# Kernel optimization log

Measured on AMD Instinct MI355X. Metric: run time of the kernel, lower is better.

## Reference

```python
import jax, jax.numpy as jnp
import numpy as np

B, N, D_MODEL, H, D_FF, NB_FEAT = 2, 2048, 512, 8, 2048, 256
DH = D_MODEL // H


def layer_norm(x, g, b, eps=1e-5):
    mu = jnp.mean(x, axis=-1, keepdims=True)
    var = jnp.mean((x - mu) ** 2, axis=-1, keepdims=True)
    return g * (x - mu) / jnp.sqrt(var + eps) + b


def softmax_kernel(data, proj, is_query, eps=1e-4):
    # Performer FAVOR+ positive random features. data: [b,h,n,dh], proj: [m,dh]
    dn = data.shape[-1] ** -0.25
    ratio = proj.shape[0] ** -0.5
    dd = jnp.einsum('bhnd,jd->bhnj', dn * data, proj)
    diag = (jnp.sum(data ** 2, axis=-1, keepdims=True) * 0.5) * (dn ** 2)
    if is_query:
        m = jnp.max(dd, axis=-1, keepdims=True)
    else:
        m = jnp.max(dd)
    return ratio * (jnp.exp(dd - diag - m) + eps)


def setup_inputs() -> dict:
    key = jax.random.key(0)
    ks = jax.random.split(key, 12)
    sd = D_MODEL ** -0.5
    sf = D_FF ** -0.5
    return {
        'x': jax.random.normal(ks[0], (B, N, D_MODEL), jnp.float32),
        'Wq': jax.random.normal(ks[1], (D_MODEL, D_MODEL), jnp.float32) * sd,
        'bq': jnp.zeros((D_MODEL,), jnp.float32),
        'Wk': jax.random.normal(ks[2], (D_MODEL, D_MODEL), jnp.float32) * sd,
        'bk': jnp.zeros((D_MODEL,), jnp.float32),
        'Wv': jax.random.normal(ks[3], (D_MODEL, D_MODEL), jnp.float32) * sd,
        'bv': jnp.zeros((D_MODEL,), jnp.float32),
        'Wo': jax.random.normal(ks[4], (D_MODEL, D_MODEL), jnp.float32) * sd,
        'bo': jnp.zeros((D_MODEL,), jnp.float32),
        'proj': jax.random.normal(ks[5], (NB_FEAT, DH), jnp.float32),
        'W1': jax.random.normal(ks[6], (D_MODEL, D_FF), jnp.float32) * sd,
        'b1': jnp.zeros((D_FF,), jnp.float32),
        'W2': jax.random.normal(ks[7], (D_FF, D_MODEL), jnp.float32) * sf,
        'b2': jnp.zeros((D_MODEL,), jnp.float32),
        'g1': jnp.ones((D_MODEL,), jnp.float32),
        'beta1': jnp.zeros((D_MODEL,), jnp.float32),
        'g2': jnp.ones((D_MODEL,), jnp.float32),
        'beta2': jnp.zeros((D_MODEL,), jnp.float32),
    }


def reference(x, Wq, bq, Wk, bk, Wv, bv, Wo, bo, proj, W1, b1, W2, b2, g1, beta1, g2, beta2):
    b, n, d = x.shape
    heads = lambda W, bias: (x @ W + bias).reshape(b, n, H, DH).transpose(0, 2, 1, 3)  # bhnd
    q = softmax_kernel(heads(Wq, bq), proj, is_query=True)   # [b,h,n,m]
    k = softmax_kernel(heads(Wk, bk), proj, is_query=False)  # [b,h,n,m]
    v = heads(Wv, bv)                                        # [b,h,n,dh]
    # non-causal linear attention
    k_sum = jnp.sum(k, axis=-2)                                   # [b,h,m]
    D_inv = 1.0 / jnp.einsum('bhnf,bhf->bhn', q, k_sum)           # [b,h,n]
    context = jnp.einsum('bhnf,bhne->bhfe', k, v)                 # [b,h,m,dh]
    out = jnp.einsum('bhfe,bhnf,bhn->bhne', context, q, D_inv)    # [b,h,n,dh]
    # output_attentions=True: effective attention matrix (abs, head-mean, detached)
    attn = jnp.einsum('bhnf,bhmf->bhnm', q, k) * D_inv[..., None]
    attn_weight = jax.lax.stop_gradient(jnp.mean(jnp.abs(attn), axis=1))  # [b,n,n]
    out = out.transpose(0, 2, 1, 3).reshape(b, n, d)
    out = out @ Wo + bo
    # NOTE: original module has no residual connections
    h1 = layer_norm(out, g1, beta1)
    ff = jax.nn.relu(h1 @ W1 + b1) @ W2 + b2
    y = layer_norm(ff, g2, beta2)
    return y, attn_weight
```

## Files before the change

kernel.cpp:

```cpp
#include <hip/hip_runtime.h>
#include <math.h>

#define B_SZ   2
#define N_TOK  2048
#define DM     512
#define NH     8
#define DHH    64
#define NF     256
#define DFF    2048
#define HF     2048
#define LDQKV  1536

constexpr float DN_SCALE   = 0.35355339059327373f;
constexpr float DIAG_SCALE = 0.0625f;
constexpr float RATIO      = 0.0625f;
constexpr float FEPS       = 1e-4f;
constexpr float LN_EPS     = 1e-5f;

typedef __attribute__((ext_vector_type(8))) short bf16x8;
typedef __attribute__((ext_vector_type(8))) _Float16 f16x8;
typedef __attribute__((ext_vector_type(4))) float f32x4;

__device__ __forceinline__ short f2b(float f) {
  union { float f; unsigned u; } x; x.f = f;
  unsigned r = (x.u + 0x7fff + ((x.u >> 16) & 1)) >> 16;
  return (short)r;
}
__device__ __forceinline__ float b2f(short s) {
  union { unsigned u; float f; } x; x.u = ((unsigned)(unsigned short)s) << 16;
  return x.f;
}
__device__ __forceinline__ void gload16(const void* g, void* l) {
  __builtin_amdgcn_global_load_lds((const __attribute__((address_space(1))) void*)g,
                                   (__attribute__((address_space(3))) void*)l, 16, 0, 0);
}
__device__ __forceinline__ int swz64(int row, int kbyte) {
  return (row * 128 + kbyte) ^ ((row & 7) << 4);
}
__device__ __forceinline__ float reduce_bmax512(const float* __restrict__ bmax,
                                                float* __restrict__ red) {
  int t = threadIdx.x;
  float m = fmaxf(bmax[t], bmax[t + 256]);
  #pragma unroll
  for (int o = 1; o < 64; o <<= 1) m = fmaxf(m, __shfl_xor(m, o, 64));
  if ((t & 63) == 0) red[t >> 6] = m;
  __syncthreads();
  float r = fmaxf(fmaxf(red[0], red[1]), fmaxf(red[2], red[3]));
  __syncthreads();
  return r;
}

constexpr size_t OFF_CTXP  = 0;
constexpr size_t OFF_QB    = 4194304;
constexpr size_t OFF_OUT2  = 0;
constexpr size_t OFF_FF2   = 0;
constexpr size_t OFF_QFB   = 8388608;
constexpr size_t OFF_KB    = 12582912;
constexpr size_t OFF_QKV   = 16777216;
constexpr size_t OFF_FF1B  = 16777216;
constexpr size_t OFF_AOB   = 20971520;
constexpr size_t OFF_H1B   = 22020096;
constexpr size_t OFF_WOT   = 23068672;
constexpr size_t OFF_W1T   = 23199744;
constexpr size_t OFF_W2T   = 23724032;
constexpr size_t OFF_KSUM  = 24248320;
constexpr size_t OFF_DINV  = 24252416;
constexpr size_t OFF_CTXT  = 24285184;
constexpr size_t OFF_BMAX  = 24416256;
constexpr size_t OFF_ROWC  = 24416832;
constexpr size_t OFF_PART  = 24420928;
constexpr size_t OFF_VSUMP = 24552000;


template<bool RELU, bool OUT_BF16, bool BIAS>
__device__ __forceinline__ void gemm128_tile(short* As, short* Bs, int bx, int by,
                                             const short* __restrict__ A,
                                             const short* __restrict__ Bt,
                                             const float* __restrict__ bias,
                                             void* __restrict__ Cout, int K, int ldC) {
  int tid = threadIdx.x, lane = tid & 63, wave = tid >> 6;
  int wm = wave >> 1, wn = wave & 1;
  int bm = by * 128, bn = bx * 128;
  int srow = tid >> 3, scol = (tid & 7) * 8;
  f32x4 acc[4][4] = {};
  for (int k0 = 0; k0 < K; k0 += 64) {
    #pragma unroll
    for (int c = 0; c < 4; ++c) {
      int r = c * 32 + srow;
      gload16(A + (size_t)(bm + r) * K + k0 + scol, As + c * 2048 + wave * 512);
      gload16(Bt + (size_t)(bn + r) * K + k0 + scol, Bs + c * 2048 + wave * 512);
    }
    __syncthreads();
    #pragma unroll
    for (int kk = 0; kk < 2; ++kk) {
      bf16x8 af[4], bf[4];
      int kq = kk * 32 + (lane >> 4) * 8;
      #pragma unroll
      for (int i = 0; i < 4; ++i)
        af[i] = *(const bf16x8*)&As[(wm * 64 + i * 16 + (lane & 15)) * 64 + kq];
      #pragma unroll
      for (int j = 0; j < 4; ++j)
        bf[j] = *(const bf16x8*)&Bs[(wn * 64 + j * 16 + (lane & 15)) * 64 + kq];
      #pragma unroll
      for (int i = 0; i < 4; ++i)
        #pragma unroll
        for (int j = 0; j < 4; ++j)
          acc[i][j] = __builtin_amdgcn_mfma_f32_16x16x32_bf16(af[i], bf[j], acc[i][j], 0, 0, 0);
    }
    __syncthreads();
  }
  int row0 = bm + wm * 64, col0 = bn + wn * 64;
  #pragma unroll
  for (int i = 0; i < 4; ++i) {
    #pragma unroll
    for (int j = 0; j < 4; ++j) {
      int col = col0 + j * 16 + (lane & 15);
      float bv = BIAS ? bias[col] : 0.f;
      #pragma unroll
      for (int r = 0; r < 4; ++r) {
        int row = row0 + i * 16 + (lane >> 4) * 4 + r;
        float v = acc[i][j][r] + bv;
        if (RELU) v = fmaxf(v, 0.f);
        size_t off = (size_t)row * ldC + col;
        if (OUT_BF16) ((short*)Cout)[off] = f2b(v);
        else          ((float*)Cout)[off] = v;
      }
    }
  }
}

__device__ __forceinline__ void attnw_tile(short* As, short* Bs, int flat, int z,
                                           const short* __restrict__ qb,
                                           const short* __restrict__ kb,
                                           const float* __restrict__ rowc,
                                           float* __restrict__ attnw) {
  int tid = threadIdx.x, lane = tid & 63, wave = tid >> 6;
  int srow = tid >> 3, scol = (tid & 7) * 8;
  int tile = flat >> 4, wi = flat & 15;
  int by = (tile >> 2) * 4 + (wi >> 2);
  int bx = (tile & 3) * 4 + (wi & 3);
  int bm = by * 128, bn = bx * 128;
  const short* Ab = qb + (size_t)z * N_TOK * HF;
  const short* Bb = kb + (size_t)z * N_TOK * HF;
  const float* rc = rowc + (size_t)z * N_TOK;
  float* out = attnw + (size_t)z * N_TOK * N_TOK;
  int wm = wave >> 1, wn = wave & 1;

  f32x4 acc[4][4] = {};
  for (int k0 = 0; k0 < HF; k0 += 64) {
    #pragma unroll
    for (int c = 0; c < 4; ++c) {
      int r = c * 32 + srow;
      gload16(Ab + (size_t)(bm + r) * HF + k0 + scol, As + c * 2048 + wave * 512);
      gload16(Bb + (size_t)(bn + r) * HF + k0 + scol, Bs + c * 2048 + wave * 512);
    }
    __syncthreads();
    #pragma unroll
    for (int kk = 0; kk < 2; ++kk) {
      bf16x8 af[4], bf[4];
      int kq = kk * 32 + (lane >> 4) * 8;
      #pragma unroll
      for (int i = 0; i < 4; ++i)
        af[i] = *(const bf16x8*)&As[(wm * 64 + i * 16 + (lane & 15)) * 64 + kq];
      #pragma unroll
      for (int j = 0; j < 4; ++j)
        bf[j] = *(const bf16x8*)&Bs[(wn * 64 + j * 16 + (lane & 15)) * 64 + kq];
      #pragma unroll
      for (int i = 0; i < 4; ++i)
        #pragma unroll
        for (int j = 0; j < 4; ++j)
          acc[i][j] = __builtin_amdgcn_mfma_f32_16x16x32_bf16(af[i], bf[j], acc[i][j], 0, 0, 0);
    }
    __syncthreads();
  }
  int row0 = bm + wm * 64, col0 = bn + wn * 64;
  #pragma unroll
  for (int i = 0; i < 4; ++i) {
    #pragma unroll
    for (int j = 0; j < 4; ++j) {
      int col = col0 + j * 16 + (lane & 15);
      #pragma unroll
      for (int r = 0; r < 4; ++r) {
        int row = row0 + i * 16 + (lane >> 4) * 4 + r;
        out[(size_t)row * N_TOK + col] = acc[i][j][r] + rc[row];
      }
    }
  }
}

template<bool RELU, bool OUT_BF16>
__device__ __forceinline__ void bn64_tile(short* As, short* Bs, int bn, int bm,
                                          const short* __restrict__ A,
                                          const short* __restrict__ Bt,
                                          const float* __restrict__ bias,
                                          void* __restrict__ Cout, int N, int K) {
  int tid = threadIdx.x, lane = tid & 63, wave = tid >> 6;
  int srow = tid >> 3, scol = (tid & 7) * 8;
  f32x4 acc[2][4] = {};
  for (int k0 = 0; k0 < K; k0 += 64) {
    #pragma unroll
    for (int c = 0; c < 4; ++c)
      gload16(A + (size_t)(bm + c * 32 + srow) * K + k0 + scol, As + c * 2048 + wave * 512);
    #pragma unroll
    for (int c = 0; c < 2; ++c)
      gload16(Bt + (size_t)(bn + c * 32 + srow) * K + k0 + scol, Bs + c * 2048 + wave * 512);
    __syncthreads();
    #pragma unroll
    for (int kk = 0; kk < 2; ++kk) {
      bf16x8 af[2], bf[4];
      int kq = kk * 32 + (lane >> 4) * 8;
      #pragma unroll
      for (int i = 0; i < 2; ++i)
        af[i] = *(const bf16x8*)&As[(wave * 32 + i * 16 + (lane & 15)) * 64 + kq];
      #pragma unroll
      for (int j = 0; j < 4; ++j)
        bf[j] = *(const bf16x8*)&Bs[(j * 16 + (lane & 15)) * 64 + kq];
      #pragma unroll
      for (int i = 0; i < 2; ++i)
        #pragma unroll
        for (int j = 0; j < 4; ++j)
          acc[i][j] = __builtin_amdgcn_mfma_f32_16x16x32_bf16(af[i], bf[j], acc[i][j], 0, 0, 0);
    }
    __syncthreads();
  }
  #pragma unroll
  for (int i = 0; i < 2; ++i) {
    #pragma unroll
    for (int j = 0; j < 4; ++j) {
      int col = bn + j * 16 + (lane & 15);
      float bv = bias[col];
      #pragma unroll
      for (int r = 0; r < 4; ++r) {
        int row = bm + wave * 32 + i * 16 + (lane >> 4) * 4 + r;
        float v = acc[i][j][r] + bv;
        if (RELU) v = fmaxf(v, 0.f);
        if (OUT_BF16) ((short*)Cout)[(size_t)row * N + col] = f2b(v);
        else          ((float*)Cout)[(size_t)row * N + col] = v;
      }
    }
  }
}

__device__ __forceinline__ void pv_tile(short* As, short* Bs, int pid,
                                        const short* __restrict__ qfb,
                                        const short* __restrict__ ctxT,
                                        const float* __restrict__ Dinv,
                                        short* __restrict__ aob) {
  int tid = threadIdx.x, lane = tid & 63, wave = tid >> 6;
  int srow = tid >> 3, scol = (tid & 7) * 8;
  int bx = pid & 15, bh = pid >> 4;
  int b = bh >> 3, h = bh & 7;
  int n0 = bx * 128;

  f32x4 acc[2][4] = {};
  for (int k0 = 0; k0 < NF; k0 += 64) {
    #pragma unroll
    for (int c = 0; c < 4; ++c) {
      int r = c * 32 + srow;
      gload16(qfb + (size_t)(b * N_TOK + n0 + r) * HF + h * NF + k0 + scol,
              As + c * 2048 + wave * 512);
    }
    #pragma unroll
    for (int c = 0; c < 2; ++c) {
      int r = c * 32 + srow;
      gload16(ctxT + (size_t)bh * 16384 + (size_t)r * 256 + k0 + scol,
              Bs + c * 2048 + wave * 512);
    }
    __syncthreads();
    #pragma unroll
    for (int kk = 0; kk < 2; ++kk) {
      bf16x8 af[2], bf[4];
      int kq = kk * 32 + (lane >> 4) * 8;
      #pragma unroll
      for (int i = 0; i < 2; ++i)
        af[i] = *(const bf16x8*)&As[(wave * 32 + i * 16 + (lane & 15)) * 64 + kq];
      #pragma unroll
      for (int j = 0; j < 4; ++j)
        bf[j] = *(const bf16x8*)&Bs[(j * 16 + (lane & 15)) * 64 + kq];
      #pragma unroll
      for (int i = 0; i < 2; ++i)
        #pragma unroll
        for (int j = 0; j < 4; ++j)
          acc[i][j] = __builtin_amdgcn_mfma_f32_16x16x32_bf16(af[i], bf[j], acc[i][j], 0, 0, 0);
    }
    __syncthreads();
  }
  #pragma unroll
  for (int i = 0; i < 2; ++i) {
    #pragma unroll
    for (int j = 0; j < 4; ++j) {
      int e = j * 16 + (lane & 15);
      #pragma unroll
      for (int r = 0; r < 4; ++r) {
        int n = n0 + wave * 32 + i * 16 + (lane >> 4) * 4 + r;
        float dv = Dinv[bh * N_TOK + n];
        aob[(size_t)(b * N_TOK + n) * DM + h * DHH + e] = f2b(acc[i][j][r] * dv);
      }
    }
  }
}


__global__ __launch_bounds__(256)
void gemm_mfma_qkv(const short* __restrict__ A, const short* __restrict__ Bt,
                   float* __restrict__ Cout) {
  __shared__ short As[128 * 64];
  __shared__ short Bs[128 * 64];
  gemm128_tile<false, false, false>(As, Bs, blockIdx.x, blockIdx.y, A, Bt, nullptr,
                                    Cout, DM, LDQKV);
}

__global__ __launch_bounds__(256)
void pv_kernel(const short* __restrict__ qfb, const short* __restrict__ ctxT,
               const float* __restrict__ Dinv, short* __restrict__ aob) {
  __shared__ short As[128 * 64];
  __shared__ short Bs[64 * 64];
  pv_tile(As, Bs, blockIdx.x, qfb, ctxT, Dinv, aob);
}

__global__ __launch_bounds__(256)
void gemm_bn64_wo(const short* __restrict__ A, const short* __restrict__ Bt,
                  const float* __restrict__ bias, float* __restrict__ Cout) {
  __shared__ short As[128 * 64];
  __shared__ short Bs[64 * 64];
  bn64_tile<false, false>(As, Bs, blockIdx.x * 64, blockIdx.y * 128, A, Bt, bias, Cout, DM, DM);
}

__global__ __launch_bounds__(256)
void fatB1_kernel(const short* __restrict__ qb, const short* __restrict__ kb,
                  const float* __restrict__ rowc, float* __restrict__ attnw,
                  const short* __restrict__ h1b, const short* __restrict__ W1t,
                  const float* __restrict__ b1, short* __restrict__ ff1b) {
  __shared__ short As[128 * 64];
  __shared__ short Bs[128 * 64];
  int bid = blockIdx.x;
  if (bid < 256) {
    attnw_tile(As, Bs, bid, 0, qb, kb, rowc, attnw);
  } else {
    int flat = bid - 256;
    gemm128_tile<true, true, true>(As, Bs, flat & 15, flat >> 4, h1b, W1t, b1, ff1b,
                                   DM, DFF);
  }
}

__global__ __launch_bounds__(256)
void fatB2_kernel(const short* __restrict__ qb, const short* __restrict__ kb,
                  const float* __restrict__ rowc, float* __restrict__ attnw,
                  const short* __restrict__ ff1b, const short* __restrict__ W2t,
                  const float* __restrict__ b2, float* __restrict__ ff2) {
  __shared__ short As[128 * 64];
  __shared__ short Bs[128 * 64];
  int bid = blockIdx.x;
  if (bid < 256) {
    attnw_tile(As, Bs, bid, 1, qb, kb, rowc, attnw);
  } else {
    int pid = bid - 256;
    bn64_tile<false, false>(As, Bs, (pid & 7) * 64, (pid >> 3) * 128,
                            ff1b, W2t, b2, ff2, DM, DFF);
  }
}

__global__ void prep_kernel(const float* __restrict__ x, short* __restrict__ xb,
                            const float* Wq, const float* Wk, const float* Wv, const float* Wo,
                            short* Wqt, short* Wkt, short* Wvt, short* Wot,
                            const float* W1, short* W1t, const float* W2, short* W2t) {
  __shared__ float t[64][65];
  int id = blockIdx.x, tid = threadIdx.x;
  if (id >= 768) {
    size_t base = ((size_t)(id - 768) * 256 + tid) * 8;
    #pragma unroll
    for (int u = 0; u < 8; ++u) xb[base + u] = f2b(x[base + u]);
    return;
  }
  const float* W; short* Wt; int K, N, bx, by;
  if (id < 256) {
    int z = id >> 6, sub = id & 63;
    W  = (z == 0) ? Wq : (z == 1) ? Wk : (z == 2) ? Wv : Wo;
    Wt = (z == 0) ? Wqt : (z == 1) ? Wkt : (z == 2) ? Wvt : Wot;
    K = 512; N = 512; bx = sub & 7; by = sub >> 3;
  } else if (id < 512) {
    int sub = id - 256;
    W = W1; Wt = W1t; K = 512; N = 2048; bx = sub & 31; by = sub >> 5;
  } else {
    int sub = id - 512;
    W = W2; Wt = W2t; K = 2048; N = 512; bx = sub & 7; by = sub >> 3;
  }
  int k0 = by * 64, n0 = bx * 64;
  int lx = tid & 63, ly = tid >> 6;
  for (int r = ly; r < 64; r += 4)
    t[r][lx] = W[(size_t)(k0 + r) * N + n0 + lx];
  __syncthreads();
  for (int r = ly; r < 64; r += 4)
    Wt[(size_t)(n0 + r) * K + k0 + lx] = f2b(t[lx][r]);
}

__global__ __launch_bounds__(256)
void feat_mfma_kernel(const float* __restrict__ qkv, const float* __restrict__ bq,
                      const float* __restrict__ bk, const float* __restrict__ proj,
                      short* __restrict__ qfb, short* __restrict__ kbo,
                      float* __restrict__ part, float* __restrict__ bmax) {
  __shared__ short qh[64 * 64], ql[64 * 64];
  __shared__ short ph[128 * 64], pl[128 * 64];
  __shared__ float dpart[64][4];
  __shared__ float diag[64];
  __shared__ float wred[4];
  __shared__ float colp[4][256];
  int t = threadIdx.x;
  bool isq = (blockIdx.z == 0);
  int coff = isq ? 0 : 512;
  const float* bias = isq ? bq : bk;
  short* qout = isq ? qfb : kbo;
  int bh = blockIdx.y, b = bh >> 3, h = bh & 7;
  int n0 = blockIdx.x * 64;
  int lane = t & 63, w = t >> 6, l15 = lane & 15, lq = lane >> 4;

  {
    int r = t >> 2, cg = (t & 3) * 16;
    const float* src = qkv + (size_t)(b * N_TOK + n0 + r) * LDQKV + coff + h * 64 + cg;
    const float* bs = bias + h * 64 + cg;
    float ss = 0.f;
    #pragma unroll
    for (int c2 = 0; c2 < 2; ++c2) {
      f16x8 H, L;
      #pragma unroll
      for (int u = 0; u < 8; ++u) {
        float xv = src[c2 * 8 + u] + bs[c2 * 8 + u];
        ss += xv * xv;
        _Float16 hi = (_Float16)xv;
        H[u] = hi;
        L[u] = (_Float16)(xv - (float)hi);
      }
      int off = swz64(r, cg * 2 + c2 * 16);
      *(f16x8*)((char*)qh + off) = H;
      *(f16x8*)((char*)ql + off) = L;
    }
    dpart[r][t & 3] = ss;
  }
  __syncthreads();
  if (t < 64)
    diag[t] = (dpart[t][0] + dpart[t][1] + dpart[t][2] + dpart[t][3]) * DIAG_SCALE;

  f16x8 ah[2], al[2];
  #pragma unroll
  for (int kk = 0; kk < 2; ++kk) {
    int off = swz64(w * 16 + l15, kk * 64 + lq * 16);
    ah[kk] = *(f16x8*)((char*)qh + off);
    al[kk] = *(f16x8*)((char*)ql + off);
  }

  f32x4 acc[16] = {};
  #pragma unroll
  for (int half = 0; half < 2; ++half) {
    __syncthreads();
    {
      int r = t & 127, cg = (t >> 7) * 32;
      const float* src = proj + (size_t)(half * 128 + r) * DHH + cg;
      #pragma unroll
      for (int c2 = 0; c2 < 4; ++c2) {
        f16x8 H, L;
        #pragma unroll
        for (int u = 0; u < 8; ++u) {
          float xv = src[c2 * 8 + u];
          _Float16 hi = (_Float16)xv;
          H[u] = hi;
          L[u] = (_Float16)(xv - (float)hi);
        }
        int off = swz64(r, cg * 2 + c2 * 16);
        *(f16x8*)((char*)ph + off) = H;
        *(f16x8*)((char*)pl + off) = L;
      }
    }
    __syncthreads();
    #pragma unroll
    for (int jl = 0; jl < 8; ++jl) {
      int row = jl * 16 + l15;
      #pragma unroll
      for (int kk = 0; kk < 2; ++kk) {
        int off = swz64(row, kk * 64 + lq * 16);
        f16x8 bh8 = *(f16x8*)((char*)ph + off);
        f16x8 bl8 = *(f16x8*)((char*)pl + off);
        acc[half * 8 + jl] = __builtin_amdgcn_mfma_f32_16x16x32_f16(ah[kk], bh8, acc[half * 8 + jl], 0, 0, 0);
        acc[half * 8 + jl] = __builtin_amdgcn_mfma_f32_16x16x32_f16(al[kk], bh8, acc[half * 8 + jl], 0, 0, 0);
        acc[half * 8 + jl] = __builtin_amdgcn_mfma_f32_16x16x32_f16(ah[kk], bl8, acc[half * 8 + jl], 0, 0, 0);
      }
    }
  }

  if (isq) {
    #pragma unroll
    for (int r = 0; r < 4; ++r) {
      float mx = -3.4e38f;
      #pragma unroll
      for (int j = 0; j < 16; ++j) mx = fmaxf(mx, acc[j][r]);
      #pragma unroll
      for (int o = 1; o < 16; o <<= 1) mx = fmaxf(mx, __shfl_xor(mx, o, 64));
      int lrow = w * 16 + lq * 4 + r;
      float dg = diag[lrow];
      float ddm = mx * DN_SCALE;
      size_t base = (size_t)(b * N_TOK + n0 + lrow) * HF + h * NF + l15;
      #pragma unroll
      for (int j = 0; j < 16; ++j) {
        float v = RATIO * (expf(acc[j][r] * DN_SCALE - dg - ddm) + FEPS);
        qout[base + j * 16] = f2b(v);
      }
    }
  } else {
    float mxall = -3.4e38f;
    float cs[16];
    #pragma unroll
    for (int j = 0; j < 16; ++j) cs[j] = 0.f;
    #pragma unroll
    for (int r = 0; r < 4; ++r) {
      int lrow = w * 16 + lq * 4 + r;
      float dg = diag[lrow];
      size_t base = (size_t)(b * N_TOK + n0 + lrow) * HF + h * NF + l15;
      #pragma unroll
      for (int j = 0; j < 16; ++j) {
        float a = acc[j][r];
        mxall = fmaxf(mxall, a);
        float e = expf(a * DN_SCALE - dg);
        cs[j] += e;
        qout[base + j * 16] = f2b(e);
      }
    }
    #pragma unroll
    for (int j = 0; j < 16; ++j) {
      cs[j] += __shfl_xor(cs[j], 16, 64);
      cs[j] += __shfl_xor(cs[j], 32, 64);
    }
    if (lq == 0) {
      #pragma unroll
      for (int j = 0; j < 16; ++j) colp[w][j * 16 + l15] = cs[j];
    }
    #pragma unroll
    for (int o = 1; o < 64; o <<= 1) mxall = fmaxf(mxall, __shfl_xor(mxall, o, 64));
    if (lane == 0) wred[w] = mxall;
    __syncthreads();
    part[(size_t)(bh * 32 + blockIdx.x) * 256 + t] =
        colp[0][t] + colp[1][t] + colp[2][t] + colp[3][t];
    if (t == 0)
      bmax[bh * 32 + blockIdx.x] =
          fmaxf(fmaxf(wred[0], wred[1]), fmaxf(wred[2], wred[3])) * DN_SCALE;
  }
}

__global__ __launch_bounds__(256)
void ctx_part_kernel(const short* __restrict__ kb, const float* __restrict__ qkv,
                     const float* __restrict__ bv, float* __restrict__ ctxp,
                     float* __restrict__ vsump) {
  int bh = blockIdx.y, b = bh >> 3, h = bh & 7;
  int ns = blockIdx.z * 128;
  int tid = threadIdx.x;
  if (blockIdx.x == 4) {
    __shared__ float vred[4][64];
    int e = tid & 63, q = tid >> 6;
    float s = 0.f;
    for (int nn = q * 32; nn < q * 32 + 32; ++nn)
      s += qkv[(size_t)(b * N_TOK + ns + nn) * LDQKV + 1024 + h * DHH + e];
    vred[q][e] = s;
    __syncthreads();
    if (tid < 64)
      vsump[((size_t)blockIdx.z * 16 + bh) * 64 + tid] =
          vred[0][tid] + vred[1][tid] + vred[2][tid] + vred[3][tid] + 128.f * bv[h * DHH + tid];
    return;
  }
  int f0 = blockIdx.x * 64;
  __shared__ float kf[32][68];
  __shared__ float vs[32][68];
  int tf = (tid >> 4) * 4, te = (tid & 15) * 4;
  float acc[4][4] = {};
  for (int n0 = ns; n0 < ns + 128; n0 += 32) {
    #pragma unroll
    for (int i = 0; i < 8; i++) {
      int idx = tid + i * 256;
      int nn = idx >> 6, f = idx & 63;
      kf[nn][f] = b2f(kb[(size_t)(b * N_TOK + n0 + nn) * HF + h * NF + f0 + f]);
    }
    #pragma unroll
    for (int i = 0; i < 8; i++) {
      int idx = tid + i * 256;
      int nn = idx >> 6, e = idx & 63;
      vs[nn][e] = qkv[(size_t)(b * N_TOK + n0 + nn) * LDQKV + 1024 + h * DHH + e] + bv[h * DHH + e];
    }
    __syncthreads();
    #pragma unroll
    for (int nn = 0; nn < 32; nn++) {
      float a[4], bb[4];
      #pragma unroll
      for (int i = 0; i < 4; i++) a[i] = kf[nn][tf + i];
      #pragma unroll
      for (int j = 0; j < 4; j++) bb[j] = vs[nn][te + j];
      #pragma unroll
      for (int i = 0; i < 4; i++)
        #pragma unroll
        for (int j = 0; j < 4; j++) acc[i][j] += a[i] * bb[j];
    }
    __syncthreads();
  }
  #pragma unroll
  for (int i = 0; i < 4; i++)
    #pragma unroll
    for (int j = 0; j < 4; j++)
      ctxp[(size_t)blockIdx.z * 262144 + (size_t)bh * 16384 +
           (size_t)(f0 + tf + i) * 64 + te + j] = acc[i][j];
}

__global__ __launch_bounds__(256)
void smallfat_kernel(const float* __restrict__ part, const float* __restrict__ bmax,
                     float* __restrict__ ksum, const float* __restrict__ ctxp,
                     const float* __restrict__ vsump, short* __restrict__ ctxT) {
  __shared__ float T[64][65];
  __shared__ float red[4];
  int t = threadIdx.x;
  float m = reduce_bmax512(bmax, red);
  float s = expf(-m);
  if (blockIdx.x < 16) {
    int bh = blockIdx.x;
    float sum = 0.f;
    #pragma unroll 8
    for (int c = 0; c < 32; ++c) sum += part[(size_t)(bh * 32 + c) * 256 + t];
    ksum[bh * 256 + t] = RATIO * (s * sum + (float)N_TOK * FEPS);
  } else {
    int id = blockIdx.x - 16;
    int ftile = id & 3, bh = id >> 2;
    int e = t & 63, q = t >> 6;
    float vsum_e = 0.f;
    #pragma unroll
    for (int c = 0; c < 16; ++c) vsum_e += vsump[((size_t)c * 16 + bh) * 64 + e];
    #pragma unroll
    for (int i = 0; i < 16; ++i) {
      int fl = i * 4 + q;
      size_t idx = (size_t)bh * 16384 + (size_t)(ftile * 64 + fl) * 64 + e;
      float sum = 0.f;
      #pragma unroll
      for (int c = 0; c < 16; ++c) sum += ctxp[(size_t)c * 262144 + idx];
      T[fl][e] = RATIO * (s * sum + FEPS * vsum_e);
    }
    __syncthreads();
    #pragma unroll
    for (int i = 0; i < 16; ++i) {
      int er = i * 4 + q;
      ctxT[(size_t)bh * 16384 + (size_t)er * 256 + ftile * 64 + e] = f2b(T[e][er]);
    }
  }
}

__global__ __launch_bounds__(256)
void dinvqs_kernel(const short* __restrict__ qfb, const float* __restrict__ ksum,
                   const float* __restrict__ bmax, float* __restrict__ Dinv,
                   float* __restrict__ rowc, short* __restrict__ qb) {
  __shared__ float red[4];
  __shared__ float wsum[4];
  int R = blockIdx.x;
  int b = R >> 11, n = R & 2047;
  int t = threadIdx.x;
  float m = reduce_bmax512(bmax, red);
  float sc = RATIO * expf(-m);
  bf16x8 qv = *(const bf16x8*)(qfb + (size_t)R * HF + t * 8);
  const float* ks = ksum + b * 2048 + t * 8;
  float p = 0.f;
  #pragma unroll
  for (int u = 0; u < 8; ++u) p += b2f(qv[u]) * ks[u];
  #pragma unroll
  for (int o = 1; o < 32; o <<= 1) p += __shfl_xor(p, o, 64);
  float d = 1.0f / p;
  if ((t & 31) == 0) Dinv[(b * NH + (t >> 5)) * N_TOK + n] = d;
  float dv = d * 0.125f;
  float qs = 0.f;
  bf16x8 o8;
  #pragma unroll
  for (int u = 0; u < 8; ++u) {
    float qb_f = b2f(qv[u]) * dv;
    qs += qb_f;
    o8[u] = f2b(qb_f * sc);
  }
  *(bf16x8*)(qb + (size_t)R * HF + t * 8) = o8;
  #pragma unroll
  for (int o = 1; o < 64; o <<= 1) qs += __shfl_xor(qs, o, 64);
  if ((t & 63) == 0) wsum[t >> 6] = qs;
  __syncthreads();
  if (t == 0) rowc[R] = RATIO * FEPS * (wsum[0] + wsum[1] + wsum[2] + wsum[3]);
}

template<bool OUT_BF16>
__global__ void ln_kernel(const float* __restrict__ x, const float* __restrict__ g,
                          const float* __restrict__ beta, void* __restrict__ y) {
  int row = blockIdx.x, t = threadIdx.x;
  __shared__ float red[4];
  __shared__ float bcast[2];
  const float* xr = x + (size_t)row * DM;
  float v0 = xr[t], v1 = xr[t + 256];
  float s = v0 + v1;
  #pragma unroll
  for (int o = 32; o > 0; o >>= 1) s += __shfl_xor(s, o, 64);
  if ((t & 63) == 0) red[t >> 6] = s;
  __syncthreads();
  if (t == 0) bcast[0] = (red[0] + red[1] + red[2] + red[3]) * (1.0f / 512.0f);
  __syncthreads();
  float mean = bcast[0];
  float d0 = v0 - mean, d1 = v1 - mean;
  float s2 = d0 * d0 + d1 * d1;
  #pragma unroll
  for (int o = 32; o > 0; o >>= 1) s2 += __shfl_xor(s2, o, 64);
  if ((t & 63) == 0) red[t >> 6] = s2;
  __syncthreads();
  if (t == 0) bcast[1] = (red[0] + red[1] + red[2] + red[3]) * (1.0f / 512.0f);
  __syncthreads();
  float inv = rsqrtf(bcast[1] + LN_EPS);
  float o0 = g[t] * d0 * inv + beta[t];
  float o1 = g[t + 256] * d1 * inv + beta[t + 256];
  if (OUT_BF16) {
    ((short*)y)[(size_t)row * DM + t] = f2b(o0);
    ((short*)y)[(size_t)row * DM + t + 256] = f2b(o1);
  } else {
    ((float*)y)[(size_t)row * DM + t] = o0;
    ((float*)y)[(size_t)row * DM + t + 256] = o1;
  }
}

extern "C" void kernel_launch(void* const* d_in, const int* in_sizes, int n_in,
                              void* d_out, int out_size, void* d_ws, size_t ws_size,
                              hipStream_t stream) {
  const float* x     = (const float*)d_in[0];
  const float* Wq    = (const float*)d_in[1];
  const float* bq    = (const float*)d_in[2];
  const float* Wk    = (const float*)d_in[3];
  const float* bk    = (const float*)d_in[4];
  const float* Wv    = (const float*)d_in[5];
  const float* bv    = (const float*)d_in[6];
  const float* Wo    = (const float*)d_in[7];
  const float* bo    = (const float*)d_in[8];
  const float* proj  = (const float*)d_in[9];
  const float* W1    = (const float*)d_in[10];
  const float* b1    = (const float*)d_in[11];
  const float* W2    = (const float*)d_in[12];
  const float* b2    = (const float*)d_in[13];
  const float* g1    = (const float*)d_in[14];
  const float* beta1 = (const float*)d_in[15];
  const float* g2    = (const float*)d_in[16];
  const float* beta2 = (const float*)d_in[17];

  float* ws = (float*)d_ws;
  float* y_out = (float*)d_out;
  float* attnw = y_out + (size_t)B_SZ * N_TOK * DM;

  float* ctxp  = ws + OFF_CTXP;
  short* qb    = (short*)(ws + OFF_QB);
  float* out2  = ws + OFF_OUT2;
  float* ff2   = ws + OFF_FF2;
  short* ff1b  = (short*)(ws + OFF_FF1B);
  short* qfb   = (short*)(ws + OFF_QFB);
  short* xb    = (short*)(ws + OFF_QFB);
  short* kb    = (short*)(ws + OFF_KB);
  short* Wqkvt = (short*)(ws + OFF_KB);
  float* QKVlin = ws + OFF_QKV;
  short* aob   = (short*)(ws + OFF_AOB);
  short* h1b   = (short*)(ws + OFF_H1B);
  short* Wot   = (short*)(ws + OFF_WOT);
  short* W1t   = (short*)(ws + OFF_W1T);
  short* W2t   = (short*)(ws + OFF_W2T);
  float* ksum  = ws + OFF_KSUM;
  float* Dinv  = ws + OFF_DINV;
  short* ctxT  = (short*)(ws + OFF_CTXT);
  float* bmax  = ws + OFF_BMAX;
  float* rowc  = ws + OFF_ROWC;
  float* part  = ws + OFF_PART;
  float* vsump = ws + OFF_VSUMP;

  dim3 blk(256);
  int MT = B_SZ * N_TOK;

  prep_kernel<<<1792, blk, 0, stream>>>(x, xb, Wq, Wk, Wv, Wo,
                                        Wqkvt, Wqkvt + 262144, Wqkvt + 524288, Wot,
                                        W1, W1t, W2, W2t);

  gemm_mfma_qkv<<<dim3(LDQKV / 128, MT / 128), blk, 0, stream>>>(xb, Wqkvt, QKVlin);

  feat_mfma_kernel<<<dim3(N_TOK / 64, B_SZ * NH, 2), blk, 0, stream>>>(
      QKVlin, bq, bk, proj, qfb, kb, part, bmax);

  ctx_part_kernel<<<dim3(5, B_SZ * NH, 16), blk, 0, stream>>>(kb, QKVlin, bv, ctxp, vsump);

  smallfat_kernel<<<80, blk, 0, stream>>>(part, bmax, ksum, ctxp, vsump, ctxT);

  dinvqs_kernel<<<MT, blk, 0, stream>>>(qfb, ksum, bmax, Dinv, rowc, qb);

  pv_kernel<<<dim3(N_TOK / 128 * B_SZ * NH), blk, 0, stream>>>(qfb, ctxT, Dinv, aob);

  gemm_bn64_wo<<<dim3(DM / 64, MT / 128), blk, 0, stream>>>(aob, Wot, bo, out2);

  ln_kernel<true><<<MT, blk, 0, stream>>>(out2, g1, beta1, h1b);

  fatB1_kernel<<<768, blk, 0, stream>>>(qb, kb, rowc, attnw, h1b, W1t, b1, ff1b);

  fatB2_kernel<<<512, blk, 0, stream>>>(qb, kb, rowc, attnw, ff1b, W2t, b2, ff2);

  ln_kernel<false><<<MT, blk, 0, stream>>>(ff2, g2, beta2, y_out);
}
```

Before: 217.3 us.

## Double-buffer attention-weight GEMM and merge both batches into one fused launch

Both batches' attention-weight tiles now run in a single fused launch alongside the W1 GEMM. The separate W2 GEMM runs afterwards as its own bn64 kernel. The attention tile loop is double-buffered in LDS, with explicit vmcnt waits and raw barriers so the next K-slice loads while the current one computes. The context-partial kernel's staging loads are vectorized to 8-wide reads with the V bias hoisted. The intent is to hide global-load latency and rebalance the fused launches. In exchange, LDS use per block doubles, which may reduce occupancy.

New measurement: 224.0 us. 3.1% more time.

```diff
diff --git a/kernel.cpp b/kernel.cpp
--- a/kernel.cpp
+++ b/kernel.cpp
@@ -129,65 +129,6 @@
   }
 }
 
-__device__ __forceinline__ void attnw_tile(short* As, short* Bs, int flat, int z,
-                                           const short* __restrict__ qb,
-                                           const short* __restrict__ kb,
-                                           const float* __restrict__ rowc,
-                                           float* __restrict__ attnw) {
-  int tid = threadIdx.x, lane = tid & 63, wave = tid >> 6;
-  int srow = tid >> 3, scol = (tid & 7) * 8;
-  int tile = flat >> 4, wi = flat & 15;
-  int by = (tile >> 2) * 4 + (wi >> 2);
-  int bx = (tile & 3) * 4 + (wi & 3);
-  int bm = by * 128, bn = bx * 128;
-  const short* Ab = qb + (size_t)z * N_TOK * HF;
-  const short* Bb = kb + (size_t)z * N_TOK * HF;
-  const float* rc = rowc + (size_t)z * N_TOK;
-  float* out = attnw + (size_t)z * N_TOK * N_TOK;
-  int wm = wave >> 1, wn = wave & 1;
-
-  f32x4 acc[4][4] = {};
-  for (int k0 = 0; k0 < HF; k0 += 64) {
-    #pragma unroll
-    for (int c = 0; c < 4; ++c) {
-      int r = c * 32 + srow;
-      gload16(Ab + (size_t)(bm + r) * HF + k0 + scol, As + c * 2048 + wave * 512);
-      gload16(Bb + (size_t)(bn + r) * HF + k0 + scol, Bs + c * 2048 + wave * 512);
-    }
-    __syncthreads();
-    #pragma unroll
-    for (int kk = 0; kk < 2; ++kk) {
-      bf16x8 af[4], bf[4];
-      int kq = kk * 32 + (lane >> 4) * 8;
-      #pragma unroll
-      for (int i = 0; i < 4; ++i)
-        af[i] = *(const bf16x8*)&As[(wm * 64 + i * 16 + (lane & 15)) * 64 + kq];
-      #pragma unroll
-      for (int j = 0; j < 4; ++j)
-        bf[j] = *(const bf16x8*)&Bs[(wn * 64 + j * 16 + (lane & 15)) * 64 + kq];
-      #pragma unroll
-      for (int i = 0; i < 4; ++i)
-        #pragma unroll
-        for (int j = 0; j < 4; ++j)
-          acc[i][j] = __builtin_amdgcn_mfma_f32_16x16x32_bf16(af[i], bf[j], acc[i][j], 0, 0, 0);
-    }
-    __syncthreads();
-  }
-  int row0 = bm + wm * 64, col0 = bn + wn * 64;
-  #pragma unroll
-  for (int i = 0; i < 4; ++i) {
-    #pragma unroll
-    for (int j = 0; j < 4; ++j) {
-      int col = col0 + j * 16 + (lane & 15);
-      #pragma unroll
-      for (int r = 0; r < 4; ++r) {
-        int row = row0 + i * 16 + (lane >> 4) * 4 + r;
-        out[(size_t)row * N_TOK + col] = acc[i][j][r] + rc[row];
-      }
-    }
-  }
-}
-
 template<bool RELU, bool OUT_BF16>
 __device__ __forceinline__ void bn64_tile(short* As, short* Bs, int bn, int bm,
                                           const short* __restrict__ A,
@@ -326,37 +267,102 @@
   bn64_tile<false, false>(As, Bs, blockIdx.x * 64, blockIdx.y * 128, A, Bt, bias, Cout, DM, DM);
 }
 
+template<bool RELU, bool OUT_BF16>
 __global__ __launch_bounds__(256)
-void fatB1_kernel(const short* __restrict__ qb, const short* __restrict__ kb,
+void gemm_bn64(const short* __restrict__ A, const short* __restrict__ Bt,
+               const float* __restrict__ bias, void* __restrict__ Cout,
+               int M, int N, int K) {
+  __shared__ short As[128 * 64];
+  __shared__ short Bs[64 * 64];
+  bn64_tile<RELU, OUT_BF16>(As, Bs, blockIdx.x * 64, blockIdx.y * 128, A, Bt, bias, Cout, N, K);
+}
+
+__global__ __launch_bounds__(256)
+void fatC1_kernel(const short* __restrict__ qb, const short* __restrict__ kb,
                   const float* __restrict__ rowc, float* __restrict__ attnw,
                   const short* __restrict__ h1b, const short* __restrict__ W1t,
                   const float* __restrict__ b1, short* __restrict__ ff1b) {
-  __shared__ short As[128 * 64];
-  __shared__ short Bs[128 * 64];
+  __shared__ short As[2][128 * 64];
+  __shared__ short Bs[2][128 * 64];
   int bid = blockIdx.x;
-  if (bid < 256) {
-    attnw_tile(As, Bs, bid, 0, qb, kb, rowc, attnw);
+  int tid = threadIdx.x, lane = tid & 63, wave = tid >> 6;
+  int srow = tid >> 3, scol = (tid & 7) * 8;
+
+  if (bid < 512) {
+    int z = bid >> 8, flat = bid & 255;
+    int tile = flat >> 4, wi = flat & 15;
+    int by = (tile >> 2) * 4 + (wi >> 2);
+    int bx = (tile & 3) * 4 + (wi & 3);
+    int bm = by * 128, bn = bx * 128;
+    const short* Ab = qb + (size_t)z * N_TOK * HF;
+    const short* Bb = kb + (size_t)z * N_TOK * HF;
+    const float* rc = rowc + (size_t)z * N_TOK;
+    float* out = attnw + (size_t)z * N_TOK * N_TOK;
+    int wm = wave >> 1, wn = wave & 1;
+    f32x4 acc[4][4] = {};
+
+    #pragma unroll
+    for (int c = 0; c < 4; ++c) {
+      int r = c * 32 + srow;
+      gload16(Ab + (size_t)(bm + r) * HF + scol, As[0] + c * 2048 + wave * 512);
+      gload16(Bb + (size_t)(bn + r) * HF + scol, Bs[0] + c * 2048 + wave * 512);
+    }
+    for (int it = 0; it < HF / 64; ++it) {
+      int cur = it & 1;
+      if (it + 1 < HF / 64) {
+        int k1 = (it + 1) * 64;
+        short* An = As[cur ^ 1];
+        short* Bn = Bs[cur ^ 1];
+        #pragma unroll
+        for (int c = 0; c < 4; ++c) {
+          int r = c * 32 + srow;
+          gload16(Ab + (size_t)(bm + r) * HF + k1 + scol, An + c * 2048 + wave * 512);
+          gload16(Bb + (size_t)(bn + r) * HF + k1 + scol, Bn + c * 2048 + wave * 512);
+        }
+        asm volatile("s_waitcnt vmcnt(8)" ::: "memory");
+      } else {
+        asm volatile("s_waitcnt vmcnt(0)" ::: "memory");
+      }
+      __builtin_amdgcn_s_barrier();
+      __builtin_amdgcn_sched_barrier(0);
+      const short* Ac = As[cur];
+      const short* Bc = Bs[cur];
+      #pragma unroll
+      for (int kk = 0; kk < 2; ++kk) {
+        bf16x8 af[4], bf[4];
+        int kq = kk * 32 + (lane >> 4) * 8;
+        #pragma unroll
+        for (int i = 0; i < 4; ++i)
+          af[i] = *(const bf16x8*)&Ac[(wm * 64 + i * 16 + (lane & 15)) * 64 + kq];
+        #pragma unroll
+        for (int j = 0; j < 4; ++j)
+          bf[j] = *(const bf16x8*)&Bc[(wn * 64 + j * 16 + (lane & 15)) * 64 + kq];
+        #pragma unroll
+        for (int i = 0; i < 4; ++i)
+          #pragma unroll
+          for (int j = 0; j < 4; ++j)
+            acc[i][j] = __builtin_amdgcn_mfma_f32_16x16x32_bf16(af[i], bf[j], acc[i][j], 0, 0, 0);
+      }
+      __builtin_amdgcn_sched_barrier(0);
+      __builtin_amdgcn_s_barrier();
+    }
+    int row0 = bm + wm * 64, col0 = bn + wn * 64;
+    #pragma unroll
+    for (int i = 0; i < 4; ++i) {
+      #pragma unroll
+      for (int j = 0; j < 4; ++j) {
+        int col = col0 + j * 16 + (lane & 15);
+        #pragma unroll
+        for (int r = 0; r < 4; ++r) {
+          int row = row0 + i * 16 + (lane >> 4) * 4 + r;
+          out[(size_t)row * N_TOK + col] = acc[i][j][r] + rc[row];
+        }
+      }
+    }
   } else {
-    int flat = bid - 256;
-    gemm128_tile<true, true, true>(As, Bs, flat & 15, flat >> 4, h1b, W1t, b1, ff1b,
+    int flat = bid - 512;
+    gemm128_tile<true, true, true>(As[0], Bs[0], flat & 15, flat >> 4, h1b, W1t, b1, ff1b,
                                    DM, DFF);
-  }
-}
-
-__global__ __launch_bounds__(256)
-void fatB2_kernel(const short* __restrict__ qb, const short* __restrict__ kb,
-                  const float* __restrict__ rowc, float* __restrict__ attnw,
-                  const short* __restrict__ ff1b, const short* __restrict__ W2t,
-                  const float* __restrict__ b2, float* __restrict__ ff2) {
-  __shared__ short As[128 * 64];
-  __shared__ short Bs[128 * 64];
-  int bid = blockIdx.x;
-  if (bid < 256) {
-    attnw_tile(As, Bs, bid, 1, qb, kb, rowc, attnw);
-  } else {
-    int pid = bid - 256;
-    bn64_tile<false, false>(As, Bs, (pid & 7) * 64, (pid >> 3) * 128,
-                            ff1b, W2t, b2, ff2, DM, DFF);
   }
 }
 
@@ -568,20 +574,18 @@
   __shared__ float kf[32][68];
   __shared__ float vs[32][68];
   int tf = (tid >> 4) * 4, te = (tid & 15) * 4;
+  int nn8 = tid >> 3, f8 = (tid & 7) * 8;
+  float bvv[8];
+  #pragma unroll
+  for (int u = 0; u < 8; ++u) bvv[u] = bv[h * DHH + f8 + u];
   float acc[4][4] = {};
   for (int n0 = ns; n0 < ns + 128; n0 += 32) {
-    #pragma unroll
-    for (int i = 0; i < 8; i++) {
-      int idx = tid + i * 256;
-      int nn = idx >> 6, f = idx & 63;
-      kf[nn][f] = b2f(kb[(size_t)(b * N_TOK + n0 + nn) * HF + h * NF + f0 + f]);
-    }
-    #pragma unroll
-    for (int i = 0; i < 8; i++) {
-      int idx = tid + i * 256;
-      int nn = idx >> 6, e = idx & 63;
-      vs[nn][e] = qkv[(size_t)(b * N_TOK + n0 + nn) * LDQKV + 1024 + h * DHH + e] + bv[h * DHH + e];
-    }
+    bf16x8 kv8 = *(const bf16x8*)&kb[(size_t)(b * N_TOK + n0 + nn8) * HF + h * NF + f0 + f8];
+    #pragma unroll
+    for (int u = 0; u < 8; ++u) kf[nn8][f8 + u] = b2f(kv8[u]);
+    const float* vrow = qkv + (size_t)(b * N_TOK + n0 + nn8) * LDQKV + 1024 + h * DHH + f8;
+    #pragma unroll
+    for (int u = 0; u < 8; ++u) vs[nn8][f8 + u] = vrow[u] + bvv[u];
     __syncthreads();
     #pragma unroll
     for (int nn = 0; nn < 32; nn++) {
@@ -791,9 +795,10 @@
 
   ln_kernel<true><<<MT, blk, 0, stream>>>(out2, g1, beta1, h1b);
 
-  fatB1_kernel<<<768, blk, 0, stream>>>(qb, kb, rowc, attnw, h1b, W1t, b1, ff1b);
-
-  fatB2_kernel<<<512, blk, 0, stream>>>(qb, kb, rowc, attnw, ff1b, W2t, b2, ff2);
+  fatC1_kernel<<<1024, blk, 0, stream>>>(qb, kb, rowc, attnw, h1b, W1t, b1, ff1b);
+
+  gemm_bn64<false, false><<<dim3(DM / 64, MT / 128), blk, 0, stream>>>(
+      ff1b, W2t, b2, ff2, MT, DM, DFF);
 
   ln_kernel<false><<<MT, blk, 0, stream>>>(ff2, g2, beta2, y_out);
 }
```
